# Kernel tuning notes

Measured on AMD Instinct MI355X. Metric: run time of the kernel, lower is better.

## Reference

```python
import jax, jax.numpy as jnp
import numpy as np

NUM_HEADS = 12


def setup_inputs() -> dict:
    key = jax.random.key(0)
    ks = jax.random.split(key, 8)
    B, Nq, Nk, C = 4, 2048, 2048, 768
    s = 0.02
    return {
        "query": jax.random.normal(ks[0], (B, Nq, C), dtype=jnp.float32),
        "key": jax.random.normal(ks[1], (B, Nk, C), dtype=jnp.float32),
        "value": jax.random.normal(ks[2], (B, Nk, C), dtype=jnp.float32),
        "Wq": jax.random.normal(ks[3], (C, C), dtype=jnp.float32) * s,
        "Wk": jax.random.normal(ks[4], (C, C), dtype=jnp.float32) * s,
        "Wv": jax.random.normal(ks[5], (C, C), dtype=jnp.float32) * s,
        "Wo": jax.random.normal(ks[6], (C, C), dtype=jnp.float32) * s,
        "bo": jnp.zeros((C,), dtype=jnp.float32),
    }


def reference(query, key, value, Wq, Wk, Wv, Wo, bo):
    B, Nq, C = query.shape
    Nk = key.shape[1]
    H = NUM_HEADS
    Dh = C // H
    scale = Dh ** -0.5
    # nn.Linear: x @ W.T ; split heads -> [B, H, N, Dh]
    q = (query @ Wq.T).reshape(B, Nq, H, Dh).transpose(0, 2, 1, 3)
    k = (key @ Wk.T).reshape(B, Nk, H, Dh).transpose(0, 2, 1, 3)
    v = (value @ Wv.T).reshape(B, Nk, H, Dh).transpose(0, 2, 1, 3)
    # attention logits [B, H, Nq, Nk]
    attn = jnp.einsum("bhqd,bhkd->bhqk", q, k) * scale
    attn = jax.nn.softmax(attn, axis=-1)
    x = jnp.einsum("bhqk,bhkd->bhqd", attn, v)  # [B, H, Nq, Dh]
    x = x.transpose(0, 2, 1, 3).reshape(B, Nq, C)
    return x @ Wo.T + bo
```

## Files before the change

kernel.cpp:

```cpp
#include <hip/hip_runtime.h>
#include <hip/hip_bf16.h>
#include <stdint.h>

typedef unsigned short u16;
typedef unsigned int   u32;
typedef unsigned long long u64;

typedef __attribute__((ext_vector_type(8)))  short short8;
typedef __attribute__((ext_vector_type(4)))  u32   u32x4;
typedef __attribute__((ext_vector_type(4)))  float f32x4;
typedef __attribute__((ext_vector_type(16))) float f32x16;


__device__ __forceinline__ u16 f2bf(float f) {
  u32 u = __builtin_bit_cast(u32, f);
  u += 0x7FFFu + ((u >> 16) & 1u);
  return (u16)(u >> 16);
}

__device__ __forceinline__ void gload16(const void* g, void* l) {
  __builtin_amdgcn_global_load_lds((__attribute__((address_space(1))) void*)(g),
                                   (__attribute__((address_space(3))) void*)(l),
                                   16, 0, 0);
}

__device__ __forceinline__ u32 cvtpk(float lo, float hi) {
  u32 r;
  asm("v_cvt_pk_bf16_f32 %0, %1, %2" : "=v"(r) : "v"(lo), "v"(hi));
  return r;
}


__global__ __launch_bounds__(256)
void cvtw_kernel(const float* __restrict__ Wq, const float* __restrict__ Wk,
                 const float* __restrict__ Wv, const float* __restrict__ Wo,
                 u16* __restrict__ Wcat, u16* __restrict__ WoB, int n4, float qs) {
  int i = blockIdx.x * 256 + threadIdx.x;
  if (i >= n4) return;
  int y = blockIdx.y;
  const float* in = y == 0 ? Wq : y == 1 ? Wk : y == 2 ? Wv : Wo;
  u16* out = y == 0 ? Wcat : y == 1 ? (Wcat + 589824) : y == 2 ? (Wcat + 1179648) : WoB;
  float s = y == 0 ? qs : 1.f;
  float4 v = reinterpret_cast<const float4*>(in)[i];
  u64 pk = (u64)f2bf(v.x * s) | ((u64)f2bf(v.y * s) << 16)
         | ((u64)f2bf(v.z * s) << 32) | ((u64)f2bf(v.w * s) << 48);
  reinterpret_cast<u64*>(out)[i] = pk;
}

template<int MODE>
__global__ __launch_bounds__(256)
void gemm128(const float* __restrict__ Af0, const float* __restrict__ Af1,
             const float* __restrict__ Af2, const u16* __restrict__ Ab,
             const u16* __restrict__ Bw,
             u16* __restrict__ Cqk, u16* __restrict__ Vt,
             float* __restrict__ Cout, const float* __restrict__ bias) {
  constexpr int K  = 768;
  constexpr int KT = K / 32;
  constexpr int NBN = (MODE == 0) ? 18 : 6;
  __shared__ char lds[(MODE == 0) ? 49152 : 32768];
  char* A0 = lds;
  char* A1 = lds + ((MODE == 0) ? 16384 : 8192);
  char* B0 = lds + ((MODE == 0) ? 32768 : 16384);
  char* B1 = B0 + 8192;

  const int tid = threadIdx.x, lane = tid & 63, wid = tid >> 6;
  const int hw = blockIdx.x;
  const int L = (hw & 7) * (64 * NBN / 8) + (hw >> 3);
  const int bm = L / NBN, bn = L - bm * NBN;
  const int wr = wid >> 1, wc = wid & 1;

  const char* Agf = nullptr;
  const char* Ag16 = nullptr;
  if constexpr (MODE == 0) {
    const float* Asrc = (bn < 6) ? Af0 : (bn < 12) ? Af1 : Af2;
    Agf = (const char*)(Asrc + (size_t)bm * 128 * 768);
  } else {
    Ag16 = (const char*)Ab + (size_t)bm * 128 * (K * 2);
  }
  const char* Bg = (const char*)Bw + (size_t)bn * 128 * (K * 2);

  f32x4 acc[4][4];
  #pragma unroll
  for (int m = 0; m < 4; ++m)
    #pragma unroll
    for (int n = 0; n < 4; ++n)
      #pragma unroll
      for (int r = 0; r < 4; ++r) acc[m][n][r] = 0.f;

  auto stageA32 = [&](char* An, int kt) {
    if constexpr (MODE == 0) {
      #pragma unroll
      for (int j = 0; j < 4; ++j) {
        int off = j * 4096 + wid * 1024 + lane * 16;
        int row = off >> 7;
        int isl = (off & 127) ^ ((row & 7) << 4);
        gload16(Agf + (size_t)row * 3072 + kt * 128 + isl, An + off);
      }
    }
  };
  auto stageA16 = [&](char* An, int kt) {
    if constexpr (MODE == 1) {
      #pragma unroll
      for (int c = 0; c < 2; ++c) {
        int off = (c * 4 + wid) * 1024 + lane * 16;
        int row = off >> 6;
        int csw = (off & 63) ^ ((row & 3) << 4);
        gload16(Ag16 + (size_t)row * (K * 2) + kt * 64 + csw, An + off);
      }
    }
  };
  auto stageB = [&](char* Bn, int kt) {
    #pragma unroll
    for (int c = 0; c < 2; ++c) {
      int off = (c * 4 + wid) * 1024 + lane * 16;
      int row = off >> 6;
      int csw = (off & 63) ^ ((row & 3) << 4);
      gload16(Bg + (size_t)row * (K * 2) + kt * 64 + csw, Bn + off);
    }
  };

  stageA32(A0, 0);
  stageA16(A0, 0);
  stageB(B0, 0);
  __syncthreads();

  for (int kt = 0; kt < KT; ++kt) {
    const int cur = kt & 1;
    char* Ac = cur ? A1 : A0;  char* Bc = cur ? B1 : B0;
    char* An = cur ? A0 : A1;  char* Bn = cur ? B0 : B1;
    if (kt + 1 < KT) {
      stageA32(An, kt + 1);
      stageA16(An, kt + 1);
      stageB(Bn, kt + 1);
    }
    short8 af[4], bf[4];
    #pragma unroll
    for (int m = 0; m < 4; ++m) {
      int row = wr * 64 + m * 16 + (lane & 15);
      if constexpr (MODE == 0) {
        int swz = (row & 7) << 4;
        int o1 = (lane >> 4) * 32;
        const char* Ar = Ac + row * 128;
        f32x4 lo = *reinterpret_cast<const f32x4*>(Ar + (o1 ^ swz));
        f32x4 hi = *reinterpret_cast<const f32x4*>(Ar + ((o1 + 16) ^ swz));
        u32x4 pk = { cvtpk(lo[0], lo[1]), cvtpk(lo[2], lo[3]),
                     cvtpk(hi[0], hi[1]), cvtpk(hi[2], hi[3]) };
        af[m] = __builtin_bit_cast(short8, pk);
      } else {
        af[m] = *reinterpret_cast<const short8*>(
                  Ac + row * 64 + (((lane >> 4) * 16) ^ ((row & 3) << 4)));
      }
    }
    #pragma unroll
    for (int n = 0; n < 4; ++n) {
      int row = wc * 64 + n * 16 + (lane & 15);
      bf[n] = *reinterpret_cast<const short8*>(
                Bc + row * 64 + (((lane >> 4) * 16) ^ ((row & 3) << 4)));
    }
    #pragma unroll
    for (int m = 0; m < 4; ++m)
      #pragma unroll
      for (int n = 0; n < 4; ++n)
        acc[m][n] = __builtin_amdgcn_mfma_f32_16x16x32_bf16(af[m], bf[n], acc[m][n], 0, 0, 0);
    __syncthreads();
  }

  if constexpr (MODE == 0) {
    if (bn < 12) {
      #pragma unroll
      for (int m = 0; m < 4; ++m) {
        int grow0 = bm * 128 + wr * 64 + m * 16 + ((lane >> 4) << 2);
        #pragma unroll
        for (int n = 0; n < 4; ++n) {
          int col = bn * 128 + wc * 64 + n * 16 + (lane & 15);
          #pragma unroll
          for (int r = 0; r < 4; ++r)
            Cqk[(size_t)(grow0 + r) * 1536 + col] = f2bf(acc[m][n][r]);
        }
      }
    } else {
      #pragma unroll
      for (int m = 0; m < 4; ++m) {
        int grow0 = bm * 128 + wr * 64 + m * 16 + ((lane >> 4) << 2);
        int bb = grow0 >> 11, nn = grow0 & 2047;
        #pragma unroll
        for (int n = 0; n < 4; ++n) {
          int vc = (bn - 12) * 128 + wc * 64 + n * 16 + (lane & 15);
          int hid = vc >> 6, d = vc & 63;
          u64 pk = (u64)f2bf(acc[m][n][0]) | ((u64)f2bf(acc[m][n][1]) << 16)
                 | ((u64)f2bf(acc[m][n][2]) << 32) | ((u64)f2bf(acc[m][n][3]) << 48);
          *reinterpret_cast<u64*>(Vt + ((size_t)(bb * 12 + hid) * 64 + d) * 2048 + nn) = pk;
        }
      }
    }
  } else {
    #pragma unroll
    for (int m = 0; m < 4; ++m) {
      int grow0 = bm * 128 + wr * 64 + m * 16 + ((lane >> 4) << 2);
      #pragma unroll
      for (int n = 0; n < 4; ++n) {
        int col = bn * 128 + wc * 64 + n * 16 + (lane & 15);
        float bs = bias[col];
        #pragma unroll
        for (int r = 0; r < 4; ++r)
          Cout[(size_t)(grow0 + r) * 768 + col] = acc[m][n][r] + bs;
      }
    }
  }
}

__global__ __launch_bounds__(256)
void attn_fwd(const u16* __restrict__ QK, const u16* __restrict__ Vt,
              u16* __restrict__ X) {
  __shared__ char lds[32768];
  char* K0 = lds;          char* K1 = lds + 8192;
  char* V0 = lds + 16384;  char* V1 = lds + 24576;

  const int tid = threadIdx.x, lane = tid & 63, wid = tid >> 6;
  const int hw = blockIdx.x;
  const int L = (hw & 7) * 96 + (hw >> 3);
  const int bh = L >> 4, qt = L & 15;
  const int b = bh / 12, h = bh - b * 12;
  const int hh = lane >> 5;

  const char* Qg = (const char*)QK + ((size_t)(b * 2048 + qt * 128) * 1536 + h * 64) * 2;
  const char* Kg = (const char*)QK + ((size_t)(b * 2048) * 1536 + 768 + h * 64) * 2;
  const char* Vg = (const char*)Vt + ((size_t)bh * 64 * 2048) * 2;

  const int off0 = wid * 1024 + lane * 16;
  const int off1 = off0 + 4096;
  const int r0 = off0 >> 7, i0 = (off0 & 127) ^ ((r0 & 7) << 4);
  const int r1 = off1 >> 7, i1 = (off1 & 127) ^ ((r1 & 7) << 4);
  const int pb0 = (r0 >> 2) & 7, pb1 = (r1 >> 2) & 7;
  const int kr0 = (r0 & 32) | ((((pb0 & 1) << 1) | ((pb0 >> 1) & 1) | (pb0 & 4)) << 2) | (r0 & 3);
  const int kr1 = (r1 & 32) | ((((pb1 & 1) << 1) | ((pb1 >> 1) & 1) | (pb1 & 4)) << 2) | (r1 & 3);
  const size_t kso0 = (size_t)kr0 * 3072 + i0, kso1 = (size_t)kr1 * 3072 + i1;
  const size_t vso0 = (size_t)r0 * 4096 + i0, vso1 = (size_t)r1 * 4096 + i1;

  gload16(Kg + kso0, K0 + off0);
  gload16(Kg + kso1, K0 + off1);
  gload16(Vg + vso0, V0 + off0);
  gload16(Vg + vso1, V0 + off1);

  short8 qf[4];
  {
    const char* Qrow = Qg + (size_t)(wid * 32 + (lane & 31)) * 3072 + hh * 16;
    #pragma unroll
    for (int kk = 0; kk < 4; ++kk)
      qf[kk] = *reinterpret_cast<const short8*>(Qrow + kk * 32);
  }
  __syncthreads();

  f32x16 o0, o1;
  #pragma unroll
  for (int r = 0; r < 16; ++r) { o0[r] = 0.f; o1[r] = 0.f; }
  float l_run = 0.f;

  for (int t = 0; t < 32; ++t) {
    const int cur = t & 1;
    char* Kc = cur ? K1 : K0;  char* Vc = cur ? V1 : V0;
    char* Kn = cur ? K0 : K1;  char* Vn = cur ? V0 : V1;
    if (t + 1 < 32) {
      const char* Kgn = Kg + (size_t)(t + 1) * 64 * 3072;
      const char* Vgn = Vg + (size_t)(t + 1) * 128;
      gload16(Kgn + kso0, Kn + off0);
      gload16(Kgn + kso1, Kn + off1);
      gload16(Vgn + vso0, Vn + off0);
      gload16(Vgn + vso1, Vn + off1);
    }

    f32x16 sa, sb;
    #pragma unroll
    for (int r = 0; r < 16; ++r) { sa[r] = 0.f; sb[r] = 0.f; }
    {
      const int ra = lane & 31;
      const int swa = (ra & 7) << 4;
      const char* Ka = Kc + ra * 128;
      const char* Kb2 = Kc + (32 + ra) * 128;
      __builtin_amdgcn_s_setprio(1);
      #pragma unroll
      for (int kk = 0; kk < 4; ++kk) {
        int inner = (kk * 32 + hh * 16) ^ swa;
        short8 ka = *reinterpret_cast<const short8*>(Ka + inner);
        short8 kb = *reinterpret_cast<const short8*>(Kb2 + inner);
        sa = __builtin_amdgcn_mfma_f32_32x32x16_bf16(ka, qf[kk], sa, 0, 0, 0);
        sb = __builtin_amdgcn_mfma_f32_32x32x16_bf16(kb, qf[kk], sb, 0, 0, 0);
      }
      __builtin_amdgcn_s_setprio(0);
    }

    float pa[16], pb[16];
    float s0 = 0.f, s1 = 0.f, s2 = 0.f, s3 = 0.f;
    #pragma unroll
    for (int r = 0; r < 16; r += 4) {
      pa[r]     = __builtin_amdgcn_exp2f(sa[r]);     s0 += pa[r];
      pa[r + 1] = __builtin_amdgcn_exp2f(sa[r + 1]); s1 += pa[r + 1];
      pa[r + 2] = __builtin_amdgcn_exp2f(sa[r + 2]); s2 += pa[r + 2];
      pa[r + 3] = __builtin_amdgcn_exp2f(sa[r + 3]); s3 += pa[r + 3];
    }
    #pragma unroll
    for (int r = 0; r < 16; r += 4) {
      pb[r]     = __builtin_amdgcn_exp2f(sb[r]);     s0 += pb[r];
      pb[r + 1] = __builtin_amdgcn_exp2f(sb[r + 1]); s1 += pb[r + 1];
      pb[r + 2] = __builtin_amdgcn_exp2f(sb[r + 2]); s2 += pb[r + 2];
      pb[r + 3] = __builtin_amdgcn_exp2f(sb[r + 3]); s3 += pb[r + 3];
    }
    l_run += (s0 + s1) + (s2 + s3);

    short8 pf[4];
    {
      u32x4 w0 = { cvtpk(pa[0],  pa[1]),  cvtpk(pa[2],  pa[3]),
                   cvtpk(pa[4],  pa[5]),  cvtpk(pa[6],  pa[7]) };
      u32x4 w1 = { cvtpk(pa[8],  pa[9]),  cvtpk(pa[10], pa[11]),
                   cvtpk(pa[12], pa[13]), cvtpk(pa[14], pa[15]) };
      u32x4 w2 = { cvtpk(pb[0],  pb[1]),  cvtpk(pb[2],  pb[3]),
                   cvtpk(pb[4],  pb[5]),  cvtpk(pb[6],  pb[7]) };
      u32x4 w3 = { cvtpk(pb[8],  pb[9]),  cvtpk(pb[10], pb[11]),
                   cvtpk(pb[12], pb[13]), cvtpk(pb[14], pb[15]) };
      pf[0] = __builtin_bit_cast(short8, w0);
      pf[1] = __builtin_bit_cast(short8, w1);
      pf[2] = __builtin_bit_cast(short8, w2);
      pf[3] = __builtin_bit_cast(short8, w3);
    }

    {
      const int rv = lane & 31;
      const int swv = (rv & 7) << 4;
      const char* Va = Vc + rv * 128;
      const char* Vb = Vc + (32 + rv) * 128;
      __builtin_amdgcn_s_setprio(1);
      #pragma unroll
      for (int st = 0; st < 4; ++st) {
        int inner = (st * 32 + hh * 16) ^ swv;
        short8 v0 = *reinterpret_cast<const short8*>(Va + inner);
        short8 v1 = *reinterpret_cast<const short8*>(Vb + inner);
        o0 = __builtin_amdgcn_mfma_f32_32x32x16_bf16(v0, pf[st], o0, 0, 0, 0);
        o1 = __builtin_amdgcn_mfma_f32_32x32x16_bf16(v1, pf[st], o1, 0, 0, 0);
      }
      __builtin_amdgcn_s_setprio(0);
    }
    __syncthreads();
  }

  l_run += __shfl_xor(l_run, 32);

  const float invl = __builtin_amdgcn_rcpf(l_run);
  const int q = qt * 128 + wid * 32 + (lane & 31);
  u16* Xp = X + (size_t)(b * 2048 + q) * 768;
  #pragma unroll
  for (int mt = 0; mt < 2; ++mt) {
    #pragma unroll
    for (int rr = 0; rr < 4; ++rr) {
      float e0 = (mt ? o1[rr * 4 + 0] : o0[rr * 4 + 0]) * invl;
      float e1 = (mt ? o1[rr * 4 + 1] : o0[rr * 4 + 1]) * invl;
      float e2 = (mt ? o1[rr * 4 + 2] : o0[rr * 4 + 2]) * invl;
      float e3 = (mt ? o1[rr * 4 + 3] : o0[rr * 4 + 3]) * invl;
      int col = h * 64 + mt * 32 + 8 * rr + 4 * hh;
      u64 pk = (u64)f2bf(e0) | ((u64)f2bf(e1) << 16)
             | ((u64)f2bf(e2) << 32) | ((u64)f2bf(e3) << 48);
      *reinterpret_cast<u64*>(Xp + col) = pk;
    }
  }
}


extern "C" void kernel_launch(void* const* d_in, const int* in_sizes, int n_in,
                              void* d_out, int out_size, void* d_ws, size_t ws_size,
                              hipStream_t stream) {
  const float* query = (const float*)d_in[0];
  const float* key   = (const float*)d_in[1];
  const float* value = (const float*)d_in[2];
  const float* Wq    = (const float*)d_in[3];
  const float* Wk    = (const float*)d_in[4];
  const float* Wv    = (const float*)d_in[5];
  const float* Wo    = (const float*)d_in[6];
  const float* bo    = (const float*)d_in[7];

  char* ws = (char*)d_ws;
  u16* Wcat = (u16*)ws;
  u16* WoB  = (u16*)(ws + (size_t)2304 * 768 * 2);
  u16* Xq   = (u16*)(ws + (size_t)2304 * 768 * 2 + (size_t)768 * 768 * 2);
  u16* QKb  = Xq  + (size_t)8192 * 768;
  u16* VtB  = QKb + (size_t)8192 * 1536;

  const float qs = 0.125f * 1.4426950408889634f;
  cvtw_kernel<<<dim3(576, 4), 256, 0, stream>>>(Wq, Wk, Wv, Wo, Wcat, WoB, 147456, qs);

  gemm128<0><<<dim3(1152), 256, 0, stream>>>(query, key, value, nullptr, Wcat,
                                             QKb, VtB, nullptr, nullptr);
  attn_fwd<<<dim3(768), 256, 0, stream>>>(QKb, VtB, Xq);
  gemm128<1><<<dim3(384), 256, 0, stream>>>(nullptr, nullptr, nullptr, Xq, WoB,
                                            nullptr, nullptr, (float*)d_out, bo);
}
```

Measured before the change: 161.5 us.

## Convert fp32 A tiles to bf16 in registers before LDS staging in projection GEMM

```diff
diff --git a/kernel.cpp b/kernel.cpp
--- a/kernel.cpp
+++ b/kernel.cpp
@@ -29,6 +29,8 @@
   asm("v_cvt_pk_bf16_f32 %0, %1, %2" : "=v"(r) : "v"(lo), "v"(hi));
   return r;
 }
+
+__device__ __forceinline__ int bswz(int row) { return ((row >> 1) & 3) << 4; }
 
 
 __global__ __launch_bounds__(256)
@@ -57,11 +59,9 @@
   constexpr int K  = 768;
   constexpr int KT = K / 32;
   constexpr int NBN = (MODE == 0) ? 18 : 6;
-  __shared__ char lds[(MODE == 0) ? 49152 : 32768];
-  char* A0 = lds;
-  char* A1 = lds + ((MODE == 0) ? 16384 : 8192);
-  char* B0 = lds + ((MODE == 0) ? 32768 : 16384);
-  char* B1 = B0 + 8192;
+  __shared__ char lds[32768];
+  char* A0 = lds;          char* A1 = lds + 8192;
+  char* B0 = lds + 16384;  char* B1 = lds + 24576;
 
   const int tid = threadIdx.x, lane = tid & 63, wid = tid >> 6;
   const int hw = blockIdx.x;
@@ -69,15 +69,18 @@
   const int bm = L / NBN, bn = L - bm * NBN;
   const int wr = wid >> 1, wc = wid & 1;
 
-  const char* Agf = nullptr;
+  const float* Agr = nullptr;
   const char* Ag16 = nullptr;
   if constexpr (MODE == 0) {
     const float* Asrc = (bn < 6) ? Af0 : (bn < 12) ? Af1 : Af2;
-    Agf = (const char*)(Asrc + (size_t)bm * 128 * 768);
+    Agr = Asrc + (size_t)(bm * 128 + (tid >> 1)) * 768 + (tid & 1) * 16;
   } else {
     Ag16 = (const char*)Ab + (size_t)bm * 128 * (K * 2);
   }
   const char* Bg = (const char*)Bw + (size_t)bn * 128 * (K * 2);
+
+  const int arow = tid >> 1, ahf = tid & 1;
+  const int aswz = bswz(arow);
 
   f32x4 acc[4][4];
   #pragma unroll
@@ -87,15 +90,27 @@
       #pragma unroll
       for (int r = 0; r < 4; ++r) acc[m][n][r] = 0.f;
 
-  auto stageA32 = [&](char* An, int kt) {
+  f32x4 a4[4];
+  auto loadA = [&](int kt) {
     if constexpr (MODE == 0) {
       #pragma unroll
+      for (int j = 0; j < 4; ++j)
+        a4[j] = *reinterpret_cast<const f32x4*>(Agr + kt * 32 + 4 * j);
+    }
+  };
+  auto writeA = [&](char* An) {
+    if constexpr (MODE == 0) {
+      u32 c[8];
+      #pragma unroll
       for (int j = 0; j < 4; ++j) {
-        int off = j * 4096 + wid * 1024 + lane * 16;
-        int row = off >> 7;
-        int isl = (off & 127) ^ ((row & 7) << 4);
-        gload16(Agf + (size_t)row * 3072 + kt * 128 + isl, An + off);
-      }
+        c[2 * j]     = cvtpk(a4[j][0], a4[j][1]);
+        c[2 * j + 1] = cvtpk(a4[j][2], a4[j][3]);
+      }
+      u32x4 w0 = { c[0], c[1], c[2], c[3] };
+      u32x4 w1 = { c[4], c[5], c[6], c[7] };
+      char* Ar = An + arow * 64;
+      *reinterpret_cast<u32x4*>(Ar + ((ahf * 32)      ^ aswz)) = w0;
+      *reinterpret_cast<u32x4*>(Ar + ((ahf * 32 + 16) ^ aswz)) = w1;
     }
   };
   auto stageA16 = [&](char* An, int kt) {
@@ -104,7 +119,7 @@
       for (int c = 0; c < 2; ++c) {
         int off = (c * 4 + wid) * 1024 + lane * 16;
         int row = off >> 6;
-        int csw = (off & 63) ^ ((row & 3) << 4);
+        int csw = (off & 63) ^ bswz(row);
         gload16(Ag16 + (size_t)row * (K * 2) + kt * 64 + csw, An + off);
       }
     }
@@ -114,14 +129,15 @@
     for (int c = 0; c < 2; ++c) {
       int off = (c * 4 + wid) * 1024 + lane * 16;
       int row = off >> 6;
-      int csw = (off & 63) ^ ((row & 3) << 4);
+      int csw = (off & 63) ^ bswz(row);
       gload16(Bg + (size_t)row * (K * 2) + kt * 64 + csw, Bn + off);
     }
   };
 
-  stageA32(A0, 0);
+  loadA(0);
   stageA16(A0, 0);
   stageB(B0, 0);
+  writeA(A0);
   __syncthreads();
 
   for (int kt = 0; kt < KT; ++kt) {
@@ -129,7 +145,7 @@
     char* Ac = cur ? A1 : A0;  char* Bc = cur ? B1 : B0;
     char* An = cur ? A0 : A1;  char* Bn = cur ? B0 : B1;
     if (kt + 1 < KT) {
-      stageA32(An, kt + 1);
+      loadA(kt + 1);
       stageA16(An, kt + 1);
       stageB(Bn, kt + 1);
     }
@@ -137,31 +153,21 @@
     #pragma unroll
     for (int m = 0; m < 4; ++m) {
       int row = wr * 64 + m * 16 + (lane & 15);
-      if constexpr (MODE == 0) {
-        int swz = (row & 7) << 4;
-        int o1 = (lane >> 4) * 32;
-        const char* Ar = Ac + row * 128;
-        f32x4 lo = *reinterpret_cast<const f32x4*>(Ar + (o1 ^ swz));
-        f32x4 hi = *reinterpret_cast<const f32x4*>(Ar + ((o1 + 16) ^ swz));
-        u32x4 pk = { cvtpk(lo[0], lo[1]), cvtpk(lo[2], lo[3]),
-                     cvtpk(hi[0], hi[1]), cvtpk(hi[2], hi[3]) };
-        af[m] = __builtin_bit_cast(short8, pk);
-      } else {
-        af[m] = *reinterpret_cast<const short8*>(
-                  Ac + row * 64 + (((lane >> 4) * 16) ^ ((row & 3) << 4)));
-      }
+      af[m] = *reinterpret_cast<const short8*>(
+                Ac + row * 64 + (((lane >> 4) * 16) ^ bswz(row)));
     }
     #pragma unroll
     for (int n = 0; n < 4; ++n) {
       int row = wc * 64 + n * 16 + (lane & 15);
       bf[n] = *reinterpret_cast<const short8*>(
-                Bc + row * 64 + (((lane >> 4) * 16) ^ ((row & 3) << 4)));
+                Bc + row * 64 + (((lane >> 4) * 16) ^ bswz(row)));
     }
     #pragma unroll
     for (int m = 0; m < 4; ++m)
       #pragma unroll
       for (int n = 0; n < 4; ++n)
         acc[m][n] = __builtin_amdgcn_mfma_f32_16x16x32_bf16(af[m], bf[n], acc[m][n], 0, 0, 0);
+    if (kt + 1 < KT) writeA(An);
     __syncthreads();
   }
 
```

Measured after the change: 166.5 us. +3.1%, slower.
